# Optimization experiments

Measured on AMD Instinct MI355X. Metric: run time of the kernel, lower is better.

The kernel has to match this reference:

```python
import jax, jax.numpy as jnp
import numpy as np

B, T, DIM, H = 2, 2048, 1024, 16
HD = DIM // H  # head_dim = 64
ROPE_BASE = 10000.0


def setup_inputs() -> dict:
    key = jax.random.key(0)
    k1, k2, k3, k4 = jax.random.split(key, 4)
    s = 1.0 / np.sqrt(DIM)
    return {
        "x": jax.random.normal(k1, (B, T, DIM), dtype=jnp.float32),
        "Wqkv": jax.random.normal(k2, (DIM, 3 * DIM), dtype=jnp.float32) * s,
        "Wout": jax.random.normal(k3, (DIM, DIM), dtype=jnp.float32) * s,
        "bout": jax.random.normal(k4, (DIM,), dtype=jnp.float32) * 0.01,
    }


def _rotate_half(x):
    # interleaved rotation: (x0,x1,x2,x3,...) -> (-x1,x0,-x3,x2,...)
    x1 = x[..., ::2]
    x2 = x[..., 1::2]
    return jnp.stack((-x2, x1), axis=-1).reshape(x.shape)


def _rope_cos_sin(seq_len, dtype):
    inv_freq = 1.0 / (ROPE_BASE ** (jnp.arange(0, HD, 2, dtype=jnp.float32) / HD))
    t = jnp.arange(seq_len, dtype=jnp.float32)
    freqs = t[:, None] * inv_freq[None, :]          # [T, HD/2]
    emb = jnp.concatenate((freqs, freqs), axis=-1)  # [T, HD] (cat layout, as in source)
    return jnp.cos(emb).astype(dtype), jnp.sin(emb).astype(dtype)


def reference(x, Wqkv, Wout, bout):
    b, t, _ = x.shape
    qkv = x @ Wqkv                                  # [B, T, 3*DIM]
    q, k, v = jnp.split(qkv, 3, axis=-1)
    # b t (h d) -> b h t d
    reshape = lambda z: z.reshape(b, t, H, HD).transpose(0, 2, 1, 3)
    q, k, v = reshape(q), reshape(k), reshape(v)
    cos, sin = _rope_cos_sin(t, x.dtype)            # [T, HD]
    q = q * cos + _rotate_half(q) * sin
    k = k * cos + _rotate_half(k) * sin
    scale = HD ** -0.5
    scores = jnp.einsum("bhqd,bhkd->bhqk", q, k) * scale
    attn = jax.nn.softmax(scores, axis=-1)
    out = jnp.einsum("bhqk,bhkd->bhqd", attn, v)    # [B, H, T, HD]
    out = out.transpose(0, 2, 1, 3).reshape(b, t, DIM)
    return out @ Wout + bout
```

## Files before the change

kernel.cpp:

```cpp
#include <hip/hip_runtime.h>
#include <math.h>


typedef unsigned short u16;
typedef __attribute__((ext_vector_type(8))) short short8;
typedef __attribute__((ext_vector_type(4))) short short4v;
typedef __attribute__((ext_vector_type(4))) float f32x4;
typedef __attribute__((ext_vector_type(16))) float f32x16;

#define T_SEQ 2048

#if __has_builtin(__builtin_amdgcn_exp2f)
#define EXP2(x) __builtin_amdgcn_exp2f(x)
#else
#define EXP2(x) exp2f(x)
#endif

__device__ __forceinline__ float b2f(u16 u) {
    union { unsigned int i; float f; } x; x.i = ((unsigned int)u) << 16; return x.f;
}
__device__ __forceinline__ u16 f2b(float f) {
    union { float f; unsigned int i; } x; x.f = f;
    return (u16)((x.i + 0x7FFFu + ((x.i >> 16) & 1u)) >> 16);
}
__device__ __forceinline__ void gl_lds16(const u16* g, u16* l) {
    __builtin_amdgcn_global_load_lds(
        (const __attribute__((address_space(1))) unsigned int*)g,
        (__attribute__((address_space(3))) unsigned int*)l, 16, 0, 0);
}
__device__ __forceinline__ unsigned int packpair(float a, float b) {
    union { float f; unsigned int u; } xa, xb; xa.f = a; xb.f = b;
    return (xa.u >> 16) | (xb.u & 0xffff0000u);
}

__global__ __launch_bounds__(256) void setup_kernel(
    const float* __restrict__ x, const float* __restrict__ Wqkv,
    const float* __restrict__ Wout, u16* __restrict__ xb,
    u16* __restrict__ WqkvT, u16* __restrict__ WoutT,
    float* __restrict__ costab, float* __restrict__ sintab)
{
    const int bid = blockIdx.x;
    const int tid = threadIdx.x;

    if (bid < 4096) {
        int i = (bid * 256 + tid) * 4;
        float4 v = *(const float4*)(x + i);
        ushort4 w;
        w.x = f2b(v.x); w.y = f2b(v.y); w.z = f2b(v.z); w.w = f2b(v.w);
        *(ushort4*)(xb + i) = w;
        return;
    }
    if (bid < 8192) {
        const float* in; u16* out; int R, Cn, bx, by;
        if (bid < 7168) { in = Wqkv; out = WqkvT; R = 1024; Cn = 3072;
                          int id = bid - 4096; bx = id % 96; by = id / 96; }
        else            { in = Wout; out = WoutT; R = 1024; Cn = 1024;
                          int id = bid - 7168; bx = id & 31; by = id >> 5; }
        __shared__ u16 tile[32][33];
        const int tx = tid & 31, ty = tid >> 5;
        const int r0 = by * 32, c0 = bx * 32;
#pragma unroll
        for (int rr = ty; rr < 32; rr += 8)
            tile[tx][rr] = f2b(in[(size_t)(r0 + rr) * Cn + c0 + tx]);
        __syncthreads();
#pragma unroll
        for (int rr = ty; rr < 32; rr += 8)
            out[(size_t)(c0 + rr) * R + r0 + tx] = tile[rr][tx];
        return;
    }
    {
        int idx = (bid - 8192) * 256 + tid;
        int t = idx >> 6, d = idx & 63;
        const float nl32 = -0.28782313662425576f;
        float f = __expf((float)(d & 31) * nl32);
        float s, c;
        __sincosf((float)t * f, &s, &c);
        costab[idx] = c; sintab[idx] = s;
    }
}

template<int OBF>
__global__ __launch_bounds__(256) void gemm_bt_mfma(
    const u16* __restrict__ A, const u16* __restrict__ Bt,
    void* __restrict__ Cv, const float* __restrict__ bias,
    int M, int N, int K)
{
    __shared__ u16 sbuf[24576];
    u16* const As0 = sbuf;
    u16* const Bs0 = sbuf + 12288;

    const int tid = threadIdx.x;
    const int wave = tid >> 6, lane = tid & 63;
    const int col = lane & 15, quad = lane >> 4;
    const int wm = (wave & 1) * 64, wn = (wave >> 1) * 64;
    const int m0 = blockIdx.y * 128, n0 = blockIdx.x * 128;

    f32x4 acc[4][4];
#pragma unroll
    for (int i = 0; i < 4; ++i)
#pragma unroll
        for (int j = 0; j < 4; ++j) acc[i][j] = f32x4{0.f, 0.f, 0.f, 0.f};

    const int c1 = tid, c2 = tid + 256;
    const u16* a1 = A + (size_t)(m0 + (c1 >> 2)) * K + (c1 & 3) * 8;
    const u16* a2 = A + (size_t)(m0 + (c2 >> 2)) * K + (c2 & 3) * 8;
    const u16* b1 = Bt + (size_t)(n0 + (c1 >> 2)) * K + (c1 & 3) * 8;
    const u16* b2 = Bt + (size_t)(n0 + (c2 >> 2)) * K + (c2 & 3) * 8;
    const int l1 = c1 * 8, l2 = c2 * 8;

#define GST(p, ks) do { const int k0_ = (ks) * 32;                            \
        gl_lds16(a1 + k0_, As0 + (p) * 4096 + l1);                            \
        gl_lds16(a2 + k0_, As0 + (p) * 4096 + l2);                            \
        gl_lds16(b1 + k0_, Bs0 + (p) * 4096 + l1);                            \
        gl_lds16(b2 + k0_, Bs0 + (p) * 4096 + l2);                            \
    } while (0)

    const int NK = K >> 5;
    GST(0, 0);
    GST(1, 1);

    int cur = 0, prv = 2;
    for (int ks = 0; ks < NK; ++ks) {
        if (ks < NK - 1) asm volatile("s_waitcnt vmcnt(4)" ::: "memory");
        else             asm volatile("s_waitcnt vmcnt(0)" ::: "memory");
        __builtin_amdgcn_s_barrier();
        asm volatile("" ::: "memory");
        __builtin_amdgcn_sched_barrier(0);

        short8 af[4], bfr[4];
        const u16* Ap = As0 + cur * 4096;
        const u16* Bp = Bs0 + cur * 4096;
#pragma unroll
        for (int i = 0; i < 4; ++i) {
            af[i]  = *(const short8*)&Ap[(wm + i * 16 + col) * 32 + quad * 8];
            bfr[i] = *(const short8*)&Bp[(wn + i * 16 + col) * 32 + quad * 8];
        }

        if (ks < NK - 2) GST(prv, ks + 2);

        __builtin_amdgcn_s_setprio(1);
#pragma unroll
        for (int i = 0; i < 4; ++i)
#pragma unroll
            for (int j = 0; j < 4; ++j)
                acc[i][j] = __builtin_amdgcn_mfma_f32_16x16x32_bf16(
                    af[i], bfr[j], acc[i][j], 0, 0, 0);
        __builtin_amdgcn_s_setprio(0);

        prv = cur;
        cur = (cur == 2) ? 0 : cur + 1;
    }
#undef GST

    if (OBF) {
        __syncthreads();
        u16* Cs = sbuf;
#pragma unroll
        for (int j = 0; j < 4; ++j) {
            const int cl = wn + j * 16 + col;
            const float bv = bias ? bias[n0 + cl] : 0.f;
#pragma unroll
            for (int i = 0; i < 4; ++i) {
                const int rl = wm + i * 16 + quad * 4;
#pragma unroll
                for (int r = 0; r < 4; ++r)
                    Cs[(rl + r) * 136 + cl] = f2b(acc[i][j][r] + bv);
            }
        }
        __syncthreads();
        const int row = tid >> 1, half = tid & 1;
        const u16* src = Cs + row * 136 + half * 64;
        u16* dst = (u16*)Cv + (size_t)(m0 + row) * N + n0 + half * 64;
#pragma unroll
        for (int s = 0; s < 8; ++s)
            *(short8*)(dst + s * 8) = *(const short8*)(src + s * 8);
    } else {
#pragma unroll
        for (int j = 0; j < 4; ++j) {
            int n = n0 + wn + j * 16 + col;
            float bv = bias ? bias[n] : 0.f;
#pragma unroll
            for (int i = 0; i < 4; ++i) {
                int mbase = m0 + wm + i * 16 + quad * 4;
#pragma unroll
                for (int r = 0; r < 4; ++r)
                    ((float*)Cv)[(size_t)(mbase + r) * N + n] = acc[i][j][r] + bv;
            }
        }
    }
}

__global__ __launch_bounds__(256) void prep_kernel(
    const u16* __restrict__ qkvb, const float* __restrict__ costab,
    const float* __restrict__ sintab, u16* __restrict__ Qb,
    u16* __restrict__ Kb, u16* __restrict__ Vimg)
{
    __shared__ u16 Vls[64][72];

    const int tid = threadIdx.x;
    const int bh = blockIdx.y;
    const int t0 = blockIdx.x * 64;
    const int b = bh >> 4, h = bh & 15;
    const int t_loc = tid >> 2;
    const int d0 = (tid & 3) * 16;

    const int t = t0 + t_loc;
    const u16* qp = qkvb + ((size_t)(b * T_SEQ + t)) * 3072 + h * 64 + d0;

    float ct[16], st[16];
    {
        const float* cp = costab + (size_t)t * 64 + d0;
        const float* sp = sintab + (size_t)t * 64 + d0;
#pragma unroll
        for (int j = 0; j < 16; j += 4) {
            *(float4*)&ct[j] = *(const float4*)(cp + j);
            *(float4*)&st[j] = *(const float4*)(sp + j);
        }
    }

#pragma unroll
    for (int part = 0; part < 2; ++part) {
        const float sc = part ? 1.f : 0.18033688011112042f;
        const u16* src = qp + part * 1024;
        u16* dst = (part ? Kb : Qb) + ((size_t)(bh * T_SEQ + t)) * 64 + d0;
        short8 v0 = *(const short8*)(src);
        short8 v1 = *(const short8*)(src + 8);
        float f[16];
#pragma unroll
        for (int j = 0; j < 8; ++j) { f[j] = b2f((u16)v0[j]); f[8 + j] = b2f((u16)v1[j]); }
        u16 o[16];
#pragma unroll
        for (int i = 0; i < 8; ++i) {
            float e = f[2 * i], od = f[2 * i + 1];
            o[2 * i]     = f2b((e * ct[2 * i]      - od * st[2 * i]) * sc);
            o[2 * i + 1] = f2b((od * ct[2 * i + 1] + e  * st[2 * i + 1]) * sc);
        }
        *(short8*)(dst)     = *(short8*)&o[0];
        *(short8*)(dst + 8) = *(short8*)&o[8];
    }

    {
        const u16* src = qp + 2048;
        *(short8*)&Vls[t_loc][d0]     = *(const short8*)(src);
        *(short8*)&Vls[t_loc][d0 + 8] = *(const short8*)(src + 8);
    }
    __syncthreads();
    {
        const int m_  = (tid >> 7) & 1;
        const int db  = (tid >> 6) & 1;
        const int h2  = (tid >> 5) & 1;
        const int dv  = tid & 31;
        const int k0v = m_ * 16 + h2 * 8;
        const int dcol = db * 32 + dv;
        const int kt_base = blockIdx.x * 2;
#pragma unroll
        for (int ktl = 0; ktl < 2; ++ktl) {
            u16 o[8];
#pragma unroll
            for (int j = 0; j < 8; ++j)
                o[j] = Vls[ktl * 32 + k0v + j][dcol];
            u16* dst = Vimg + ((size_t)(bh * 64 + kt_base + ktl)) * 2048 + tid * 8;
            *(short8*)dst = *(short8*)&o[0];
        }
    }
}

__global__ __launch_bounds__(256, 2) void attn32_kernel(
    const u16* __restrict__ Qb, const u16* __restrict__ Kb,
    const u16* __restrict__ Vimg, u16* __restrict__ aob)
{
    __shared__ u16 Kbuf[3][2][2048];
    __shared__ u16 Vbuf[3][2][2048];

    const int tid = threadIdx.x;
    const int wave = tid >> 6, lane = tid & 63;
    const int qcol = lane & 31;
    const int hi = lane >> 5;

    const int bid = blockIdx.x;
    const int lbid = (bid & 7) * 64 + (bid >> 3);
    const int bh = lbid >> 4;
    const int qblk = lbid & 15;
    const int qrow0 = qblk * 128 + wave * 32;

    short8 qa[4];
    {
        const u16* qp = Qb + ((size_t)(bh * T_SEQ + qrow0 + qcol)) * 64 + hi * 8;
#pragma unroll
        for (int c = 0; c < 4; ++c) qa[c] = *(const short8*)(qp + c * 16);
    }

    f32x16 O0, O1;
#pragma unroll
    for (int i = 0; i < 16; ++i) { O0[i] = 0.f; O1[i] = 0.f; }
    float Lacc = 0.f;

    const u16* kg_ptr = Kb + ((size_t)bh * T_SEQ + qcol) * 64 + wave * 16 + hi * 8;
    const u16* vg_ptr = Vimg + ((size_t)bh * 64) * 2048 + tid * 8;

#define STAGE2(p, rr) do {                                                    \
        gl_lds16(kg_ptr + (size_t)(2 * (rr))     * 2048, &Kbuf[p][0][tid * 8]);\
        gl_lds16(kg_ptr + (size_t)(2 * (rr) + 1) * 2048, &Kbuf[p][1][tid * 8]);\
        gl_lds16(vg_ptr + (size_t)(2 * (rr))     * 2048, &Vbuf[p][0][tid * 8]);\
        gl_lds16(vg_ptr + (size_t)(2 * (rr) + 1) * 2048, &Vbuf[p][1][tid * 8]);\
    } while (0)

    STAGE2(0, 0);
    STAGE2(1, 1);

    int cur = 0, prv = 2;
    for (int r = 0; r < 32; ++r) {
        if (r < 31) asm volatile("s_waitcnt vmcnt(4)" ::: "memory");
        else        asm volatile("s_waitcnt vmcnt(0)" ::: "memory");
        __builtin_amdgcn_s_barrier();
        asm volatile("" ::: "memory");
        __builtin_amdgcn_sched_barrier(0);

        short8 kf[2][4], vA[2][4];
#pragma unroll
        for (int half = 0; half < 2; ++half) {
#pragma unroll
            for (int f = 0; f < 4; ++f)
                kf[half][f] = *(const short8*)&Kbuf[cur][half][(f * 64 + lane) * 8];
#pragma unroll
            for (int rg = 0; rg < 4; ++rg)
                vA[half][rg] = *(const short8*)&Vbuf[cur][half][rg * 512 + lane * 8];
        }

        if (r < 30) STAGE2(prv, r + 2);

        f32x16 sT0, sT1;
#pragma unroll
        for (int ii = 0; ii < 16; ++ii) { sT0[ii] = 0.f; sT1[ii] = 0.f; }
        __builtin_amdgcn_s_setprio(1);
#pragma unroll
        for (int c = 0; c < 4; ++c)
            sT0 = __builtin_amdgcn_mfma_f32_32x32x16_bf16(kf[0][c], qa[c], sT0, 0, 0, 0);
#pragma unroll
        for (int c = 0; c < 4; ++c)
            sT1 = __builtin_amdgcn_mfma_f32_32x32x16_bf16(kf[1][c], qa[c], sT1, 0, 0, 0);
        __builtin_amdgcn_s_setprio(0);

        {
            float pe[16];
#pragma unroll
            for (int ii = 0; ii < 16; ++ii) pe[ii] = EXP2(sT0[ii]);
#pragma unroll
            for (int g = 0; g < 4; ++g)
                Lacc += (pe[4 * g + 0] + pe[4 * g + 1]) +
                        (pe[4 * g + 2] + pe[4 * g + 3]);
            unsigned int W0 = packpair(pe[0],  pe[1]);
            unsigned int W1 = packpair(pe[2],  pe[3]);
            unsigned int W2 = packpair(pe[4],  pe[5]);
            unsigned int W3 = packpair(pe[6],  pe[7]);
            unsigned int W4 = packpair(pe[8],  pe[9]);
            unsigned int W5 = packpair(pe[10], pe[11]);
            unsigned int W6 = packpair(pe[12], pe[13]);
            unsigned int W7 = packpair(pe[14], pe[15]);
            asm volatile("v_permlane32_swap_b32 %0, %1" : "+v"(W0), "+v"(W2));
            asm volatile("v_permlane32_swap_b32 %0, %1" : "+v"(W1), "+v"(W3));
            asm volatile("v_permlane32_swap_b32 %0, %1" : "+v"(W4), "+v"(W6));
            asm volatile("v_permlane32_swap_b32 %0, %1" : "+v"(W5), "+v"(W7));
            union FU { unsigned int u[4]; short8 s; } f0, f1;
            f0.u[0] = W0; f0.u[1] = W1; f0.u[2] = W2; f0.u[3] = W3;
            f1.u[0] = W4; f1.u[1] = W5; f1.u[2] = W6; f1.u[3] = W7;
            __builtin_amdgcn_s_setprio(1);
            O0 = __builtin_amdgcn_mfma_f32_32x32x16_bf16(vA[0][0], f0.s, O0, 0, 0, 0);
            O1 = __builtin_amdgcn_mfma_f32_32x32x16_bf16(vA[0][1], f0.s, O1, 0, 0, 0);
            O0 = __builtin_amdgcn_mfma_f32_32x32x16_bf16(vA[0][2], f1.s, O0, 0, 0, 0);
            O1 = __builtin_amdgcn_mfma_f32_32x32x16_bf16(vA[0][3], f1.s, O1, 0, 0, 0);
            __builtin_amdgcn_s_setprio(0);
        }
        {
            float pe[16];
#pragma unroll
            for (int ii = 0; ii < 16; ++ii) pe[ii] = EXP2(sT1[ii]);
#pragma unroll
            for (int g = 0; g < 4; ++g)
                Lacc += (pe[4 * g + 0] + pe[4 * g + 1]) +
                        (pe[4 * g + 2] + pe[4 * g + 3]);
            unsigned int W0 = packpair(pe[0],  pe[1]);
            unsigned int W1 = packpair(pe[2],  pe[3]);
            unsigned int W2 = packpair(pe[4],  pe[5]);
            unsigned int W3 = packpair(pe[6],  pe[7]);
            unsigned int W4 = packpair(pe[8],  pe[9]);
            unsigned int W5 = packpair(pe[10], pe[11]);
            unsigned int W6 = packpair(pe[12], pe[13]);
            unsigned int W7 = packpair(pe[14], pe[15]);
            asm volatile("v_permlane32_swap_b32 %0, %1" : "+v"(W0), "+v"(W2));
            asm volatile("v_permlane32_swap_b32 %0, %1" : "+v"(W1), "+v"(W3));
            asm volatile("v_permlane32_swap_b32 %0, %1" : "+v"(W4), "+v"(W6));
            asm volatile("v_permlane32_swap_b32 %0, %1" : "+v"(W5), "+v"(W7));
            union FU { unsigned int u[4]; short8 s; } f0, f1;
            f0.u[0] = W0; f0.u[1] = W1; f0.u[2] = W2; f0.u[3] = W3;
            f1.u[0] = W4; f1.u[1] = W5; f1.u[2] = W6; f1.u[3] = W7;
            __builtin_amdgcn_s_setprio(1);
            O0 = __builtin_amdgcn_mfma_f32_32x32x16_bf16(vA[1][0], f0.s, O0, 0, 0, 0);
            O1 = __builtin_amdgcn_mfma_f32_32x32x16_bf16(vA[1][1], f0.s, O1, 0, 0, 0);
            O0 = __builtin_amdgcn_mfma_f32_32x32x16_bf16(vA[1][2], f1.s, O0, 0, 0, 0);
            O1 = __builtin_amdgcn_mfma_f32_32x32x16_bf16(vA[1][3], f1.s, O1, 0, 0, 0);
            __builtin_amdgcn_s_setprio(0);
        }

        prv = cur;
        cur = (cur == 2) ? 0 : cur + 1;
    }
#undef STAGE2

    float Lq = Lacc + __shfl(Lacc, lane ^ 32);
    float inv = 1.f / Lq;

    const int b = bh >> 4, h = bh & 15;
    u16* ab = aob + ((size_t)(b * T_SEQ + qrow0 + qcol)) * 1024 + h * 64;
#pragma unroll
    for (int g2 = 0; g2 < 4; ++g2) {
        int dd = g2 * 8 + hi * 4;
        ushort4 w0, w1;
        w0.x = f2b(O0[4 * g2 + 0] * inv); w0.y = f2b(O0[4 * g2 + 1] * inv);
        w0.z = f2b(O0[4 * g2 + 2] * inv); w0.w = f2b(O0[4 * g2 + 3] * inv);
        w1.x = f2b(O1[4 * g2 + 0] * inv); w1.y = f2b(O1[4 * g2 + 1] * inv);
        w1.z = f2b(O1[4 * g2 + 2] * inv); w1.w = f2b(O1[4 * g2 + 3] * inv);
        *(ushort4*)(ab + dd)      = w0;
        *(ushort4*)(ab + 32 + dd) = w1;
    }
}

extern "C" void kernel_launch(void* const* d_in, const int* in_sizes, int n_in,
                              void* d_out, int out_size, void* d_ws, size_t ws_size,
                              hipStream_t stream)
{
    const float* x    = (const float*)d_in[0];
    const float* Wqkv = (const float*)d_in[1];
    const float* Wout = (const float*)d_in[2];
    const float* bout = (const float*)d_in[3];
    float* out = (float*)d_out;

    char* w = (char*)d_ws;
    u16* qkvb    = (u16*)(w);
    u16* xb      = (u16*)(w + 25165824);
    u16* WqkvT   = (u16*)(w + 33554432);
    u16* WoutT   = (u16*)(w + 39845888);
    u16* aob     = (u16*)(w + 41943040);
    u16* Qb      = (u16*)(w + 50331648);
    u16* Kb      = (u16*)(w + 58720256);
    u16* Vimg    = (u16*)(w + 67108864);
    float* ctab  = (float*)(w + 75497472);
    float* stab  = (float*)(w + 76021760);

    dim3 blk(256);
    setup_kernel<<<dim3(8704), blk, 0, stream>>>(x, Wqkv, Wout, xb, WqkvT, WoutT, ctab, stab);
    gemm_bt_mfma<1><<<dim3(24, 32), blk, 0, stream>>>(xb, WqkvT, qkvb, nullptr, 4096, 3072, 1024);
    prep_kernel<<<dim3(32, 32), blk, 0, stream>>>(qkvb, ctab, stab, Qb, Kb, Vimg);
    attn32_kernel<<<dim3(512), blk, 0, stream>>>(Qb, Kb, Vimg, aob);
    gemm_bt_mfma<0><<<dim3(8, 32), blk, 0, stream>>>(aob, WoutT, out, bout, 4096, 1024, 1024);
}
```

Baseline: 189.1 us.

## Fuse RoPE, Q/K head layout and V tiling into QKV GEMM epilogue

Removes the separate prep kernel and the intermediate qkv buffer by having the QKV GEMM epilogue apply RoPE and the softmax scale, then write Q/K in per-head layout and V in the tiled image layout directly from shared memory. This avoids a full write and reread of the 24 MB bf16 qkv tensor and one kernel launch. In exchange the GEMM epilogue does more work, including strided LDS reads for the V transpose and loads of the cos/sin tables.

```diff
diff --git a/kernel.cpp b/kernel.cpp
--- a/kernel.cpp
+++ b/kernel.cpp
@@ -83,7 +83,9 @@
 __global__ __launch_bounds__(256) void gemm_bt_mfma(
     const u16* __restrict__ A, const u16* __restrict__ Bt,
     void* __restrict__ Cv, const float* __restrict__ bias,
-    int M, int N, int K)
+    int M, int N, int K,
+    const float* __restrict__ ctab, const float* __restrict__ stab,
+    u16* __restrict__ Qb, u16* __restrict__ Kb, u16* __restrict__ Vimg)
 {
     __shared__ u16 sbuf[24576];
     u16* const As0 = sbuf;
@@ -152,114 +154,103 @@
     }
 #undef GST
 
-    if (OBF) {
-        __syncthreads();
-        u16* Cs = sbuf;
+    if (OBF == 0) {
 #pragma unroll
         for (int j = 0; j < 4; ++j) {
-            const int cl = wn + j * 16 + col;
-            const float bv = bias ? bias[n0 + cl] : 0.f;
+            int n = n0 + wn + j * 16 + col;
+            float bv = bias ? bias[n] : 0.f;
 #pragma unroll
             for (int i = 0; i < 4; ++i) {
-                const int rl = wm + i * 16 + quad * 4;
+                int mbase = m0 + wm + i * 16 + quad * 4;
 #pragma unroll
                 for (int r = 0; r < 4; ++r)
-                    Cs[(rl + r) * 136 + cl] = f2b(acc[i][j][r] + bv);
+                    ((float*)Cv)[(size_t)(mbase + r) * N + n] = acc[i][j][r] + bv;
             }
         }
-        __syncthreads();
+        return;
+    }
+
+    __syncthreads();
+    u16* Cs = sbuf;
+#pragma unroll
+    for (int j = 0; j < 4; ++j) {
+        const int cl = wn + j * 16 + col;
+        const float bv = (OBF == 1 && bias) ? bias[n0 + cl] : 0.f;
+#pragma unroll
+        for (int i = 0; i < 4; ++i) {
+            const int rl = wm + i * 16 + quad * 4;
+#pragma unroll
+            for (int r = 0; r < 4; ++r)
+                Cs[(rl + r) * 136 + cl] = f2b(acc[i][j][r] + bv);
+        }
+    }
+    __syncthreads();
+
+    if (OBF == 1) {
         const int row = tid >> 1, half = tid & 1;
         const u16* src = Cs + row * 136 + half * 64;
         u16* dst = (u16*)Cv + (size_t)(m0 + row) * N + n0 + half * 64;
 #pragma unroll
         for (int s = 0; s < 8; ++s)
             *(short8*)(dst + s * 8) = *(const short8*)(src + s * 8);
+        return;
+    }
+
+    if (n0 < 2048) {
+        const int row = tid >> 1, half = tid & 1;
+        const int tt = m0 + row;
+        const int b = tt >> 11, t = tt & 2047;
+        const int gcol = n0 + half * 64;
+        const int isQ = (gcol < 1024) ? 1 : 0;
+        const int h = (isQ ? gcol : (gcol - 1024)) >> 6;
+        const float sc = isQ ? 0.18033688011112042f : 1.f;
+        const u16* src = Cs + row * 136 + half * 64;
+        u16* dst = (isQ ? Qb : Kb) + ((size_t)((b * 16 + h) * T_SEQ + t)) * 64;
+        const float* cp = ctab + (size_t)t * 64;
+        const float* sp = stab + (size_t)t * 64;
+#pragma unroll
+        for (int c4 = 0; c4 < 4; ++c4) {
+            short8 v0 = *(const short8*)(src + c4 * 16);
+            short8 v1 = *(const short8*)(src + c4 * 16 + 8);
+            float f[16], ct4[16], st4[16];
+#pragma unroll
+            for (int jj = 0; jj < 8; ++jj) {
+                f[jj] = b2f((u16)v0[jj]); f[8 + jj] = b2f((u16)v1[jj]);
+            }
+#pragma unroll
+            for (int jj = 0; jj < 16; jj += 4) {
+                *(float4*)&ct4[jj] = *(const float4*)(cp + c4 * 16 + jj);
+                *(float4*)&st4[jj] = *(const float4*)(sp + c4 * 16 + jj);
+            }
+            u16 o[16];
+#pragma unroll
+            for (int i2 = 0; i2 < 8; ++i2) {
+                float e = f[2 * i2], od = f[2 * i2 + 1];
+                o[2 * i2]     = f2b((e * ct4[2 * i2]      - od * st4[2 * i2]) * sc);
+                o[2 * i2 + 1] = f2b((od * ct4[2 * i2 + 1] + e  * st4[2 * i2 + 1]) * sc);
+            }
+            *(short8*)(dst + c4 * 16)     = *(short8*)&o[0];
+            *(short8*)(dst + c4 * 16 + 8) = *(short8*)&o[8];
+        }
     } else {
-#pragma unroll
-        for (int j = 0; j < 4; ++j) {
-            int n = n0 + wn + j * 16 + col;
-            float bv = bias ? bias[n] : 0.f;
-#pragma unroll
-            for (int i = 0; i < 4; ++i) {
-                int mbase = m0 + wm + i * 16 + quad * 4;
-#pragma unroll
-                for (int r = 0; r < 4; ++r)
-                    ((float*)Cv)[(size_t)(mbase + r) * N + n] = acc[i][j][r] + bv;
-            }
-        }
-    }
-}
-
-__global__ __launch_bounds__(256) void prep_kernel(
-    const u16* __restrict__ qkvb, const float* __restrict__ costab,
-    const float* __restrict__ sintab, u16* __restrict__ Qb,
-    u16* __restrict__ Kb, u16* __restrict__ Vimg)
-{
-    __shared__ u16 Vls[64][72];
-
-    const int tid = threadIdx.x;
-    const int bh = blockIdx.y;
-    const int t0 = blockIdx.x * 64;
-    const int b = bh >> 4, h = bh & 15;
-    const int t_loc = tid >> 2;
-    const int d0 = (tid & 3) * 16;
-
-    const int t = t0 + t_loc;
-    const u16* qp = qkvb + ((size_t)(b * T_SEQ + t)) * 3072 + h * 64 + d0;
-
-    float ct[16], st[16];
-    {
-        const float* cp = costab + (size_t)t * 64 + d0;
-        const float* sp = sintab + (size_t)t * 64 + d0;
-#pragma unroll
-        for (int j = 0; j < 16; j += 4) {
-            *(float4*)&ct[j] = *(const float4*)(cp + j);
-            *(float4*)&st[j] = *(const float4*)(sp + j);
-        }
-    }
-
-#pragma unroll
-    for (int part = 0; part < 2; ++part) {
-        const float sc = part ? 1.f : 0.18033688011112042f;
-        const u16* src = qp + part * 1024;
-        u16* dst = (part ? Kb : Qb) + ((size_t)(bh * T_SEQ + t)) * 64 + d0;
-        short8 v0 = *(const short8*)(src);
-        short8 v1 = *(const short8*)(src + 8);
-        float f[16];
-#pragma unroll
-        for (int j = 0; j < 8; ++j) { f[j] = b2f((u16)v0[j]); f[8 + j] = b2f((u16)v1[j]); }
-        u16 o[16];
-#pragma unroll
-        for (int i = 0; i < 8; ++i) {
-            float e = f[2 * i], od = f[2 * i + 1];
-            o[2 * i]     = f2b((e * ct[2 * i]      - od * st[2 * i]) * sc);
-            o[2 * i + 1] = f2b((od * ct[2 * i + 1] + e  * st[2 * i + 1]) * sc);
-        }
-        *(short8*)(dst)     = *(short8*)&o[0];
-        *(short8*)(dst + 8) = *(short8*)&o[8];
-    }
-
-    {
-        const u16* src = qp + 2048;
-        *(short8*)&Vls[t_loc][d0]     = *(const short8*)(src);
-        *(short8*)&Vls[t_loc][d0 + 8] = *(const short8*)(src + 8);
-    }
-    __syncthreads();
-    {
-        const int m_  = (tid >> 7) & 1;
-        const int db  = (tid >> 6) & 1;
-        const int h2  = (tid >> 5) & 1;
-        const int dv  = tid & 31;
+        const int b = m0 >> 11;
+        const int h0 = (n0 - 2048) >> 6;
+        const int ktb = (m0 & 2047) >> 5;
+        const int m_ = (tid >> 7) & 1;
+        const int db = (tid >> 6) & 1;
+        const int h2 = (tid >> 5) & 1;
+        const int dv = tid & 31;
         const int k0v = m_ * 16 + h2 * 8;
-        const int dcol = db * 32 + dv;
-        const int kt_base = blockIdx.x * 2;
-#pragma unroll
-        for (int ktl = 0; ktl < 2; ++ktl) {
+#pragma unroll
+        for (int ph = 0; ph < 8; ++ph) {
+            const int panel = ph >> 1, hh = ph & 1;
+            const int bh = b * 16 + h0 + hh;
+            const int dcol = hh * 64 + db * 32 + dv;
             u16 o[8];
 #pragma unroll
-            for (int j = 0; j < 8; ++j)
-                o[j] = Vls[ktl * 32 + k0v + j][dcol];
-            u16* dst = Vimg + ((size_t)(bh * 64 + kt_base + ktl)) * 2048 + tid * 8;
+            for (int jj = 0; jj < 8; ++jj)
+                o[jj] = Cs[(panel * 32 + k0v + jj) * 136 + dcol];
+            u16* dst = Vimg + ((size_t)(bh * 64 + ktb + panel)) * 2048 + tid * 8;
             *(short8*)dst = *(short8*)&o[0];
         }
     }
@@ -436,7 +427,6 @@
     float* out = (float*)d_out;
 
     char* w = (char*)d_ws;
-    u16* qkvb    = (u16*)(w);
     u16* xb      = (u16*)(w + 25165824);
     u16* WqkvT   = (u16*)(w + 33554432);
     u16* WoutT   = (u16*)(w + 39845888);
@@ -449,8 +439,9 @@
 
     dim3 blk(256);
     setup_kernel<<<dim3(8704), blk, 0, stream>>>(x, Wqkv, Wout, xb, WqkvT, WoutT, ctab, stab);
-    gemm_bt_mfma<1><<<dim3(24, 32), blk, 0, stream>>>(xb, WqkvT, qkvb, nullptr, 4096, 3072, 1024);
-    prep_kernel<<<dim3(32, 32), blk, 0, stream>>>(qkvb, ctab, stab, Qb, Kb, Vimg);
+    gemm_bt_mfma<2><<<dim3(24, 32), blk, 0, stream>>>(
+        xb, WqkvT, nullptr, nullptr, 4096, 3072, 1024, ctab, stab, Qb, Kb, Vimg);
     attn32_kernel<<<dim3(512), blk, 0, stream>>>(Qb, Kb, Vimg, aob);
-    gemm_bt_mfma<0><<<dim3(8, 32), blk, 0, stream>>>(aob, WoutT, out, bout, 4096, 1024, 1024);
-}
+    gemm_bt_mfma<0><<<dim3(8, 32), blk, 0, stream>>>(
+        aob, WoutT, out, bout, 4096, 1024, 1024, nullptr, nullptr, nullptr, nullptr, nullptr);
+}
```

Measured after the change: 180.1 us. 1.05x faster.
